# Performance work log

Hardware: AMD Instinct MI355X
Metric: run time of the kernel (lower is better)

Reference implementation:

```python
import jax, jax.numpy as jnp
import numpy as np

B, L, D = 64, 512, 768
KSIZE, PAD = 3, 1
BN_EPS = 1e-5
COS_EPS = 1e-8

def _gauss_kernel(kernel_size, sigma, k):
    X = np.linspace(-k, k, kernel_size)
    x, y = np.meshgrid(X, X)
    g = 1.0 / (2 * np.pi * sigma ** 2) * np.exp(-(x ** 2 + y ** 2) / (2 * sigma ** 2))
    return g.astype(np.float32)

def setup_inputs() -> dict:
    key = jax.random.key(0)
    k1, k2, k3, k4 = jax.random.split(key, 4)
    news = jax.random.normal(k1, (B, L, D), dtype=jnp.float32)
    post = jax.random.normal(k2, (B, L, D), dtype=jnp.float32)
    gauss_kernel = jnp.asarray(_gauss_kernel(KSIZE, 2, 1))[None, None]  # (1,1,3,3), frozen
    bn_gamma = jnp.ones((1,), jnp.float32)
    bn_beta = jnp.zeros((1,), jnp.float32)
    bound = 1.0 / np.sqrt(L)
    lin_w = jax.random.uniform(k3, (L, L), jnp.float32, -bound, bound)
    lin_b = jax.random.uniform(k4, (L,), jnp.float32, -bound, bound)
    return {"news": news, "post": post, "gauss_kernel": gauss_kernel,
            "bn_gamma": bn_gamma, "bn_beta": bn_beta, "lin_w": lin_w, "lin_b": lin_b}

def reference(news, post, gauss_kernel, bn_gamma, bn_beta, lin_w, lin_b):
    # cosine similarity along feature dim (torch eps semantics)
    nn_ = jnp.maximum(jnp.linalg.norm(news, axis=-1), COS_EPS)
    np_ = jnp.maximum(jnp.linalg.norm(post, axis=-1), COS_EPS)
    cos = jnp.sum(news * post, axis=-1) / (nn_ * np_)           # (B, L)
    # the original loop writes the same cos row into every i -> broadcast
    trans = jnp.broadcast_to(cos[:, None, :], (cos.shape[0], cos.shape[1], cos.shape[1]))
    x = trans[:, None]                                           # (B,1,L,L)
    wk = jax.lax.conv_general_dilated(
        x, gauss_kernel, window_strides=(1, 1),
        padding=[(PAD, PAD), (PAD, PAD)],
        dimension_numbers=("NCHW", "OIHW", "NCHW"))             # (B,1,L,L)
    # BatchNorm2d(1) in training mode: batch stats over (N,H,W)
    mu = jnp.mean(wk)
    var = jnp.mean((wk - mu) ** 2)
    wk = (wk - mu) * jax.lax.rsqrt(var + BN_EPS) * bn_gamma[0] + bn_beta[0]
    wk = wk[:, 0]                                                # (B,L,L)
    wk = jnp.einsum("blm,nm->bln", wk, lin_w) + lin_b            # Linear over last dim
    wk = jax.nn.softmax(wk, axis=-2).sum(axis=-1)[..., None]     # (B,L,1)
    word_feat = (wk * news).mean(axis=1)                         # (B,D)
    post_feat = (wk * post).mean(axis=1)[:, None]                # (B,1,D)
    return (word_feat, post_feat)
```

## Files before the change

kernel.cpp:

```cpp
#include <hip/hip_runtime.h>
#include <math.h>

#define NB 64
#define NL 512
#define ND 768

static constexpr float kCosEps = 1e-8f;
static constexpr double kBnEps = 1e-5;

static constexpr size_t OFF_ACC = 0;
static constexpr size_t OFF_CSN = 256;
static constexpr size_t SZ_PART = (size_t)8 * NB * ND * 4;
static constexpr size_t OFF_CSP = OFF_CSN + SZ_PART;
static constexpr size_t OFF_COS = OFF_CSP + SZ_PART;
static constexpr size_t SZ_BL   = (size_t)NB * NL * 4;
static constexpr size_t OFF_HI  = OFF_COS + SZ_BL;
static constexpr size_t OFF_HT  = OFF_HI + SZ_BL;
static constexpr size_t OFF_HB  = OFF_HT + SZ_BL;
static constexpr size_t OFF_ABC = OFF_HB + SZ_BL;

__global__ __launch_bounds__(1024) void k1_cos_colsum(
    const float* __restrict__ news, const float* __restrict__ post,
    float* __restrict__ cosv, float* __restrict__ csn_part,
    float* __restrict__ csp_part)
{
    __shared__ float lds[16][ND];
    const int b    = blockIdx.x >> 3;
    const int tile = blockIdx.x & 7;
    const int tid  = threadIdx.x;
    const int wave = tid >> 6;
    const int lane = tid & 63;

    float an[12], ap[12];
#pragma unroll
    for (int k = 0; k < 12; ++k) { an[k] = 0.f; ap[k] = 0.f; }

#pragma unroll
    for (int r = 0; r < 4; ++r) {
        const int l = tile * 64 + r * 16 + wave;
        const float4* nrow = (const float4*)(news + ((size_t)b * NL + l) * ND);
        const float4* prow = (const float4*)(post + ((size_t)b * NL + l) * ND);
        float nn = 0.f, pp = 0.f, npd = 0.f;
#pragma unroll
        for (int k = 0; k < 3; ++k) {
            const float4 nv = nrow[lane + 64 * k];
            const float4 pv = prow[lane + 64 * k];
            nn  += nv.x * nv.x + nv.y * nv.y + nv.z * nv.z + nv.w * nv.w;
            pp  += pv.x * pv.x + pv.y * pv.y + pv.z * pv.z + pv.w * pv.w;
            npd += nv.x * pv.x + nv.y * pv.y + nv.z * pv.z + nv.w * pv.w;
            an[4 * k + 0] += nv.x; an[4 * k + 1] += nv.y;
            an[4 * k + 2] += nv.z; an[4 * k + 3] += nv.w;
            ap[4 * k + 0] += pv.x; ap[4 * k + 1] += pv.y;
            ap[4 * k + 2] += pv.z; ap[4 * k + 3] += pv.w;
        }
#pragma unroll
        for (int m = 32; m >= 1; m >>= 1) {
            nn  += __shfl_xor(nn, m);
            pp  += __shfl_xor(pp, m);
            npd += __shfl_xor(npd, m);
        }
        if (lane == 0) {
            const float dn = fmaxf(sqrtf(nn), kCosEps) * fmaxf(sqrtf(pp), kCosEps);
            cosv[b * NL + l] = npd / dn;
        }
    }

    float4* ldsrow = (float4*)&lds[wave][0];
#pragma unroll
    for (int k = 0; k < 3; ++k)
        ldsrow[lane + 64 * k] = make_float4(an[4 * k + 0], an[4 * k + 1],
                                            an[4 * k + 2], an[4 * k + 3]);
    __syncthreads();
    if (tid < ND) {
        float s = 0.f;
#pragma unroll
        for (int w = 0; w < 16; ++w) s += lds[w][tid];
        csn_part[((size_t)tile * NB + b) * ND + tid] = s;
    }
    __syncthreads();
#pragma unroll
    for (int k = 0; k < 3; ++k)
        ldsrow[lane + 64 * k] = make_float4(ap[4 * k + 0], ap[4 * k + 1],
                                            ap[4 * k + 2], ap[4 * k + 3]);
    __syncthreads();
    if (tid < ND) {
        float s = 0.f;
#pragma unroll
        for (int w = 0; w < 16; ++w) s += lds[w][tid];
        csp_part[((size_t)tile * NB + b) * ND + tid] = s;
    }
}

__global__ __launch_bounds__(256) void k2_conv_stats(
    const float* __restrict__ cosv, const float* __restrict__ g,
    float* __restrict__ hi, float* __restrict__ ht, float* __restrict__ hb,
    double* __restrict__ acc)
{
    __shared__ float row[NL + 2];
    __shared__ double sred[8];
    const int b   = blockIdx.x;
    const int tid = threadIdx.x;
    if (tid == 0) { row[0] = 0.f; row[NL + 1] = 0.f; }
    for (int j = tid; j < NL; j += 256) row[j + 1] = cosv[b * NL + j];
    __syncthreads();

    const float ci0 = g[0] + g[3] + g[6], ci1 = g[1] + g[4] + g[7], ci2 = g[2] + g[5] + g[8];
    const float ct0 = g[3] + g[6],        ct1 = g[4] + g[7],        ct2 = g[5] + g[8];
    const float cb0 = g[0] + g[3],        cb1 = g[1] + g[4],        cb2 = g[2] + g[5];

    double s = 0.0, s2 = 0.0;
    for (int j = tid; j < NL; j += 256) {
        const float a = row[j], c = row[j + 1], d = row[j + 2];
        const float vi = ci0 * a + ci1 * c + ci2 * d;
        const float vt = ct0 * a + ct1 * c + ct2 * d;
        const float vb = cb0 * a + cb1 * c + cb2 * d;
        hi[b * NL + j] = vi; ht[b * NL + j] = vt; hb[b * NL + j] = vb;
        s  += (double)vi * (NL - 2) + (double)vt + (double)vb;
        s2 += (double)vi * vi * (NL - 2) + (double)vt * vt + (double)vb * vb;
    }
    const int lane = tid & 63, wave = tid >> 6;
#pragma unroll
    for (int m = 32; m >= 1; m >>= 1) { s += __shfl_xor(s, m); s2 += __shfl_xor(s2, m); }
    if (lane == 0) { sred[wave] = s; sred[4 + wave] = s2; }
    __syncthreads();
    if (tid == 0) {
        atomicAdd(&acc[0], sred[0] + sred[1] + sred[2] + sred[3]);
        atomicAdd(&acc[1], sred[4] + sred[5] + sred[6] + sred[7]);
    }
}

__global__ __launch_bounds__(256) void k3_linear_softmax(
    const float* __restrict__ hi, const float* __restrict__ ht,
    const float* __restrict__ hb, const float* __restrict__ W,
    const float* __restrict__ bias, const float* __restrict__ gamma,
    const float* __restrict__ beta, const double* __restrict__ acc,
    float* __restrict__ abc)
{
    __shared__ float shi[NL], sht[NL], shb[NL];
    __shared__ float sred[12];
    const int b   = blockIdx.x;
    const int tid = threadIdx.x;

    const double N   = (double)NB * NL * NL;
    const double mu  = acc[0] / N;
    const double var = acc[1] / N - mu * mu;
    const float  sc  = gamma[0] * (float)(1.0 / sqrt(var + kBnEps));
    const float  sh  = beta[0] - (float)mu * sc;

    for (int j = tid; j < NL; j += 256) {
        shi[j] = hi[b * NL + j] * sc + sh;
        sht[j] = ht[b * NL + j] * sc + sh;
        shb[j] = hb[b * NL + j] * sc + sh;
    }
    __syncthreads();

    const float4* s4i = (const float4*)shi;
    const float4* s4t = (const float4*)sht;
    const float4* s4b = (const float4*)shb;

    float sa = 0.f, st = 0.f, sb = 0.f;
    for (int n = tid; n < NL; n += 256) {
        const float4* wr = (const float4*)(W + (size_t)n * NL);
        float zi = 0.f, zt = 0.f, zb = 0.f;
        for (int m = 0; m < NL / 4; ++m) {
            const float4 w  = wr[m];
            const float4 vi = s4i[m], vt = s4t[m], vb = s4b[m];
            zi += w.x * vi.x + w.y * vi.y + w.z * vi.z + w.w * vi.w;
            zt += w.x * vt.x + w.y * vt.y + w.z * vt.z + w.w * vt.w;
            zb += w.x * vb.x + w.y * vb.y + w.z * vb.z + w.w * vb.w;
        }
        const float bv = bias[n];
        zi += bv; zt += bv; zb += bv;
        const float M  = fmaxf(zi, fmaxf(zt, zb));
        const float ei = expf(zi - M), et = expf(zt - M), eb = expf(zb - M);
        const float r  = 1.f / ((float)(NL - 2) * ei + et + eb);
        sa += ei * r; st += et * r; sb += eb * r;
    }
    const int lane = tid & 63, wave = tid >> 6;
#pragma unroll
    for (int m = 32; m >= 1; m >>= 1) {
        sa += __shfl_xor(sa, m); st += __shfl_xor(st, m); sb += __shfl_xor(sb, m);
    }
    if (lane == 0) { sred[wave * 3] = sa; sred[wave * 3 + 1] = st; sred[wave * 3 + 2] = sb; }
    __syncthreads();
    if (tid == 0) {
        abc[b * 3 + 0] = sred[0] + sred[3] + sred[6] + sred[9];
        abc[b * 3 + 1] = sred[1] + sred[4] + sred[7] + sred[10];
        abc[b * 3 + 2] = sred[2] + sred[5] + sred[8] + sred[11];
    }
}

__global__ __launch_bounds__(256) void k4_out(
    const float* __restrict__ news, const float* __restrict__ post,
    const float* __restrict__ csn_part, const float* __restrict__ csp_part,
    const float* __restrict__ abc, float* __restrict__ out)
{
    const int idx = blockIdx.x * 256 + threadIdx.x;
    if (idx >= NB * ND) return;
    const int b = idx / ND, d = idx - b * ND;
    const float a  = abc[b * 3 + 0];
    const float ct = abc[b * 3 + 1];
    const float cb = abc[b * 3 + 2];
    float cn = 0.f, cp = 0.f;
#pragma unroll
    for (int t = 0; t < 8; ++t) {
        cn += csn_part[((size_t)t * NB + b) * ND + d];
        cp += csp_part[((size_t)t * NB + b) * ND + d];
    }
    const size_t base = (size_t)b * NL * ND;
    const float n0 = news[base + d], nL = news[base + (size_t)(NL - 1) * ND + d];
    const float p0 = post[base + d], pL = post[base + (size_t)(NL - 1) * ND + d];
    const float invL = 1.f / NL;
    out[idx]           = (a * cn + (ct - a) * n0 + (cb - a) * nL) * invL;
    out[NB * ND + idx] = (a * cp + (ct - a) * p0 + (cb - a) * pL) * invL;
}

extern "C" void kernel_launch(void* const* d_in, const int* in_sizes, int n_in,
                              void* d_out, int out_size, void* d_ws, size_t ws_size,
                              hipStream_t stream) {
    const float* news     = (const float*)d_in[0];
    const float* post     = (const float*)d_in[1];
    const float* g        = (const float*)d_in[2];
    const float* bn_gamma = (const float*)d_in[3];
    const float* bn_beta  = (const float*)d_in[4];
    const float* lin_w    = (const float*)d_in[5];
    const float* lin_b    = (const float*)d_in[6];
    float* out = (float*)d_out;
    char*  ws  = (char*)d_ws;

    double* acc = (double*)(ws + OFF_ACC);
    float* csn  = (float*)(ws + OFF_CSN);
    float* csp  = (float*)(ws + OFF_CSP);
    float* cosv = (float*)(ws + OFF_COS);
    float* hi   = (float*)(ws + OFF_HI);
    float* ht   = (float*)(ws + OFF_HT);
    float* hb   = (float*)(ws + OFF_HB);
    float* abc  = (float*)(ws + OFF_ABC);

    hipMemsetAsync(acc, 0, 2 * sizeof(double), stream);

    k1_cos_colsum<<<NB * 8, 1024, 0, stream>>>(news, post, cosv, csn, csp);
    k2_conv_stats<<<NB, 256, 0, stream>>>(cosv, g, hi, ht, hb, acc);
    k3_linear_softmax<<<NB, 256, 0, stream>>>(hi, ht, hb, lin_w, lin_b,
                                              bn_gamma, bn_beta, acc, abc);
    k4_out<<<192, 256, 0, stream>>>(news, post, csn, csp, abc, out);
}
```

Before: 87.74 us.

## Restructure cosine/colsum kernel: 512 threads, two rows in flight, LDS-transposed reductions

The first kernel now runs 512-thread blocks, each wave handling 8 rows. Each step issues loads for two rows of news and post together to raise memory-level parallelism. The per-row norm and dot reductions move from cross-lane shuffles to a padded LDS transpose reduced by 192 threads, and cos values are written from there. This is meant to raise bandwidth use and occupancy in the memory-bound pass, at the cost of more registers, a larger LDS buffer and extra syncs.

Result: slower. 167.2 us (+90.6%).

```diff
diff --git a/kernel.cpp b/kernel.cpp
--- a/kernel.cpp
+++ b/kernel.cpp
@@ -19,12 +19,17 @@
 static constexpr size_t OFF_HB  = OFF_HT + SZ_BL;
 static constexpr size_t OFF_ABC = OFF_HB + SZ_BL;
 
-__global__ __launch_bounds__(1024) void k1_cos_colsum(
+__device__ __forceinline__ float dot4(float4 a, float4 b) {
+    return a.x * b.x + a.y * b.y + a.z * b.z + a.w * b.w;
+}
+
+__global__ __launch_bounds__(512, 4) void k1_cos_colsum(
     const float* __restrict__ news, const float* __restrict__ post,
     float* __restrict__ cosv, float* __restrict__ csn_part,
     float* __restrict__ csp_part)
 {
-    __shared__ float lds[16][ND];
+    __shared__ float buf[64 * 193];
+    __shared__ float lds_s[192];
     const int b    = blockIdx.x >> 3;
     const int tile = blockIdx.x & 7;
     const int tid  = threadIdx.x;
@@ -32,62 +37,97 @@
     const int lane = tid & 63;
 
     float an[12], ap[12];
+    float nn[8], pp[8], npd[8];
 #pragma unroll
     for (int k = 0; k < 12; ++k) { an[k] = 0.f; ap[k] = 0.f; }
 
 #pragma unroll
-    for (int r = 0; r < 4; ++r) {
-        const int l = tile * 64 + r * 16 + wave;
-        const float4* nrow = (const float4*)(news + ((size_t)b * NL + l) * ND);
-        const float4* prow = (const float4*)(post + ((size_t)b * NL + l) * ND);
-        float nn = 0.f, pp = 0.f, npd = 0.f;
-#pragma unroll
-        for (int k = 0; k < 3; ++k) {
-            const float4 nv = nrow[lane + 64 * k];
-            const float4 pv = prow[lane + 64 * k];
-            nn  += nv.x * nv.x + nv.y * nv.y + nv.z * nv.z + nv.w * nv.w;
-            pp  += pv.x * pv.x + pv.y * pv.y + pv.z * pv.z + pv.w * pv.w;
-            npd += nv.x * pv.x + nv.y * pv.y + nv.z * pv.z + nv.w * pv.w;
-            an[4 * k + 0] += nv.x; an[4 * k + 1] += nv.y;
-            an[4 * k + 2] += nv.z; an[4 * k + 3] += nv.w;
-            ap[4 * k + 0] += pv.x; ap[4 * k + 1] += pv.y;
-            ap[4 * k + 2] += pv.z; ap[4 * k + 3] += pv.w;
-        }
-#pragma unroll
-        for (int m = 32; m >= 1; m >>= 1) {
-            nn  += __shfl_xor(nn, m);
-            pp  += __shfl_xor(pp, m);
-            npd += __shfl_xor(npd, m);
-        }
-        if (lane == 0) {
-            const float dn = fmaxf(sqrtf(nn), kCosEps) * fmaxf(sqrtf(pp), kCosEps);
-            cosv[b * NL + l] = npd / dn;
-        }
-    }
-
-    float4* ldsrow = (float4*)&lds[wave][0];
-#pragma unroll
-    for (int k = 0; k < 3; ++k)
-        ldsrow[lane + 64 * k] = make_float4(an[4 * k + 0], an[4 * k + 1],
-                                            an[4 * k + 2], an[4 * k + 3]);
-    __syncthreads();
-    if (tid < ND) {
+    for (int rp = 0; rp < 4; ++rp) {
+        const int ra = 2 * rp, rb = 2 * rp + 1;
+        const int la = tile * 64 + ra * 8 + wave;
+        const int lb = tile * 64 + rb * 8 + wave;
+        const float4* nra = (const float4*)(news + ((size_t)b * NL + la) * ND);
+        const float4* pra = (const float4*)(post + ((size_t)b * NL + la) * ND);
+        const float4* nrb = (const float4*)(news + ((size_t)b * NL + lb) * ND);
+        const float4* prb = (const float4*)(post + ((size_t)b * NL + lb) * ND);
+        const float4 A0 = nra[lane], A1 = nra[lane + 64], A2 = nra[lane + 128];
+        const float4 B0 = pra[lane], B1 = pra[lane + 64], B2 = pra[lane + 128];
+        const float4 C0 = nrb[lane], C1 = nrb[lane + 64], C2 = nrb[lane + 128];
+        const float4 D0 = prb[lane], D1 = prb[lane + 64], D2 = prb[lane + 128];
+
+        nn[ra]  = dot4(A0, A0) + dot4(A1, A1) + dot4(A2, A2);
+        pp[ra]  = dot4(B0, B0) + dot4(B1, B1) + dot4(B2, B2);
+        npd[ra] = dot4(A0, B0) + dot4(A1, B1) + dot4(A2, B2);
+        nn[rb]  = dot4(C0, C0) + dot4(C1, C1) + dot4(C2, C2);
+        pp[rb]  = dot4(D0, D0) + dot4(D1, D1) + dot4(D2, D2);
+        npd[rb] = dot4(C0, D0) + dot4(C1, D1) + dot4(C2, D2);
+
+        an[0] += A0.x + C0.x; an[1]  += A0.y + C0.y;
+        an[2] += A0.z + C0.z; an[3]  += A0.w + C0.w;
+        an[4] += A1.x + C1.x; an[5]  += A1.y + C1.y;
+        an[6] += A1.z + C1.z; an[7]  += A1.w + C1.w;
+        an[8] += A2.x + C2.x; an[9]  += A2.y + C2.y;
+        an[10] += A2.z + C2.z; an[11] += A2.w + C2.w;
+        ap[0] += B0.x + D0.x; ap[1]  += B0.y + D0.y;
+        ap[2] += B0.z + D0.z; ap[3]  += B0.w + D0.w;
+        ap[4] += B1.x + D1.x; ap[5]  += B1.y + D1.y;
+        ap[6] += B1.z + D1.z; ap[7]  += B1.w + D1.w;
+        ap[8] += B2.x + D2.x; ap[9]  += B2.y + D2.y;
+        ap[10] += B2.z + D2.z; ap[11] += B2.w + D2.w;
+    }
+
+#pragma unroll
+    for (int r = 0; r < 8; ++r) {
+        const int c = wave * 24 + r * 3;
+        buf[lane * 193 + c + 0] = nn[r];
+        buf[lane * 193 + c + 1] = pp[r];
+        buf[lane * 193 + c + 2] = npd[r];
+    }
+    __syncthreads();
+    if (tid < 192) {
         float s = 0.f;
 #pragma unroll
-        for (int w = 0; w < 16; ++w) s += lds[w][tid];
-        csn_part[((size_t)tile * NB + b) * ND + tid] = s;
-    }
-    __syncthreads();
-#pragma unroll
-    for (int k = 0; k < 3; ++k)
-        ldsrow[lane + 64 * k] = make_float4(ap[4 * k + 0], ap[4 * k + 1],
-                                            ap[4 * k + 2], ap[4 * k + 3]);
-    __syncthreads();
-    if (tid < ND) {
+        for (int l = 0; l < 64; ++l) s += buf[l * 193 + tid];
+        lds_s[tid] = s;
+    }
+    __syncthreads();
+
+    if (tid < 64) {
+        const int j = tid;
+        const float snn = lds_s[3 * j + 0];
+        const float spp = lds_s[3 * j + 1];
+        const float snp = lds_s[3 * j + 2];
+        const int row = (j & 7) * 8 + (j >> 3);
+        const float dn = fmaxf(sqrtf(snn), kCosEps) * fmaxf(sqrtf(spp), kCosEps);
+        cosv[b * NL + tile * 64 + row] = snp / dn;
+    }
+
+    {
+        float4* wrow = (float4*)&buf[wave * ND];
+        wrow[lane]       = make_float4(an[0], an[1], an[2], an[3]);
+        wrow[lane + 64]  = make_float4(an[4], an[5], an[6], an[7]);
+        wrow[lane + 128] = make_float4(an[8], an[9], an[10], an[11]);
+    }
+    __syncthreads();
+    for (int i = tid; i < ND; i += 512) {
         float s = 0.f;
 #pragma unroll
-        for (int w = 0; w < 16; ++w) s += lds[w][tid];
-        csp_part[((size_t)tile * NB + b) * ND + tid] = s;
+        for (int w = 0; w < 8; ++w) s += buf[w * ND + i];
+        csn_part[((size_t)tile * NB + b) * ND + i] = s;
+    }
+    __syncthreads();
+    {
+        float4* wrow = (float4*)&buf[wave * ND];
+        wrow[lane]       = make_float4(ap[0], ap[1], ap[2], ap[3]);
+        wrow[lane + 64]  = make_float4(ap[4], ap[5], ap[6], ap[7]);
+        wrow[lane + 128] = make_float4(ap[8], ap[9], ap[10], ap[11]);
+    }
+    __syncthreads();
+    for (int i = tid; i < ND; i += 512) {
+        float s = 0.f;
+#pragma unroll
+        for (int w = 0; w < 8; ++w) s += buf[w * ND + i];
+        csp_part[((size_t)tile * NB + b) * ND + i] = s;
     }
 }
 
@@ -239,7 +279,7 @@
 
     hipMemsetAsync(acc, 0, 2 * sizeof(double), stream);
 
-    k1_cos_colsum<<<NB * 8, 1024, 0, stream>>>(news, post, cosv, csn, csp);
+    k1_cos_colsum<<<NB * 8, 512, 0, stream>>>(news, post, cosv, csn, csp);
     k2_conv_stats<<<NB, 256, 0, stream>>>(cosv, g, hi, ht, hb, acc);
     k3_linear_softmax<<<NB, 256, 0, stream>>>(hi, ht, hb, lin_w, lin_b,
                                               bn_gamma, bn_beta, acc, abc);
```
